# Kernel optimization log

Hardware: AMD Instinct MI355X
Metric: run time of the kernel (lower is better)

Reference implementation:

```python
import jax, jax.numpy as jnp
import numpy as np
from jax import lax


def _pw(x, w, b):
    # pointwise conv1d (kernel_size=1) on [B,C,L]
    return jnp.einsum('oc,bcl->bol', w, x) + b[None, :, None]


def _conv(x, w, b, stride):
    y = lax.conv_general_dilated(x, w, (stride,), 'VALID',
                                 dimension_numbers=('NCH', 'OIH', 'NCH'))
    return y + b[None, :, None]


def setup_inputs() -> dict:
    key = jax.random.key(0)
    ks = jax.random.split(key, 40)
    B, L = 512, 300
    d = {}
    d['x'] = jax.random.randint(ks[0], (B, L), 0, 23)
    def w(k, shape, s=0.1):
        return jax.random.normal(k, shape, dtype=jnp.float32) * s
    d['emb'] = w(ks[1], (23, 128), 1.0)
    d['dr_w'] = w(ks[2], (64, 128)); d['dr_b'] = w(ks[3], (64,), 0.01)
    d['c1_w'] = w(ks[4], (64, 64)); d['c1_b'] = w(ks[5], (64,), 0.01)
    d['c11_w'] = w(ks[6], (64, 64)); d['c11_b'] = w(ks[7], (64,), 0.01)
    d['c12_w'] = w(ks[8], (64, 64)); d['c12_b'] = w(ks[9], (64,), 0.01)
    d['c21_w'] = w(ks[10], (64, 64)); d['c21_b'] = w(ks[11], (64,), 0.01)
    d['c22_w'] = w(ks[12], (64, 64)); d['c22_b'] = w(ks[13], (64,), 0.01)
    d['c31_w'] = w(ks[14], (64, 64)); d['c31_b'] = w(ks[15], (64,), 0.01)
    d['c32_w'] = w(ks[16], (64, 64)); d['c32_b'] = w(ks[17], (64,), 0.01)
    d['c41_w'] = w(ks[18], (64, 64)); d['c41_b'] = w(ks[19], (64,), 0.01)
    d['fc_w'] = w(ks[20], (64, 320)); d['fc_b'] = w(ks[21], (64,), 0.01)
    d['cp1_w'] = w(ks[22], (64, 64, 4)); d['cp1_b'] = w(ks[23], (64,), 0.01)
    d['cp2_w'] = w(ks[24], (64, 64, 5)); d['cp2_b'] = w(ks[25], (64,), 0.01)
    d['wt'] = w(ks[26], (64, 64)); d['wx'] = w(ks[27], (64, 64))
    d['bh'] = w(ks[28], (64,), 0.01)
    d['wa'] = w(ks[29], (64,)); d['ba'] = w(ks[30], (1,), 0.01)
    d['m1_w'] = w(ks[31], (100, 960)); d['m1_b'] = w(ks[32], (100,), 0.01)
    d['m2_w'] = w(ks[33], (1, 100)); d['m2_b'] = w(ks[34], (1,), 0.01)
    return d


def reference(x, emb, dr_w, dr_b, c1_w, c1_b, c11_w, c11_b, c12_w, c12_b,
              c21_w, c21_b, c22_w, c22_b, c31_w, c31_b, c32_w, c32_b,
              c41_w, c41_b, fc_w, fc_b, cp1_w, cp1_b, cp2_w, cp2_b,
              wt, wx, bh, wa, ba, m1_w, m1_b, m2_w, m2_b):
    h = emb[x]                                  # [B,L,128]
    h = jnp.transpose(h, (0, 2, 1))             # [B,128,L]
    r = _pw(h, dr_w, dr_b)                      # [B,64,L]
    r = _pw(r, c1_w, c1_b)
    x2 = _pw(_pw(r, c11_w, c11_b), c12_w, c12_b)
    x3 = _pw(_pw(r, c21_w, c21_b), c22_w, c22_b)
    x4 = _pw(_pw(r, c31_w, c31_b), c32_w, c32_b)
    # MaxPool1d(k=3, s=1, p=1)
    xp = jnp.pad(r, ((0, 0), (0, 0), (1, 1)), constant_values=-jnp.inf)
    p = jnp.maximum(jnp.maximum(xp[:, :, :-2], xp[:, :, 1:-1]), xp[:, :, 2:])
    x5 = _pw(p, c41_w, c41_b)
    h = jnp.concatenate([r, x2, x3, x4, x5], axis=1)   # [B,320,L]
    h = _pw(h, fc_w, fc_b)                             # [B,64,L]
    h = _conv(h, cp1_w, cp1_b, 4)                      # [B,64,75]
    a_in = jnp.transpose(h, (0, 2, 1))                 # [B,75,64]
    # additive attention emission
    qt = a_in @ wt.T                                   # Wt(inputs)
    kx = a_in @ wx.T                                   # Wx(inputs)
    hsc = jnp.tanh(qt[:, :, None, :] + kx[:, None, :, :] + bh)  # [B,75,75,64]
    e = jnp.einsum('bijd,d->bij', hsc, wa) + ba[0]     # [B,75,75]
    a = jax.nn.softmax(e, axis=-1)
    v = jnp.einsum('bij,bjd->bid', a, a_in)            # [B,75,64]
    h = jnp.transpose(v, (0, 2, 1))                    # [B,64,75]
    h = jax.nn.relu(h)
    h = _conv(h, cp2_w, cp2_b, 5)                      # [B,64,15]
    h = h.reshape(h.shape[0], -1)                      # [B,960]
    h = jax.nn.relu(h @ m1_w.T + m1_b)
    return h @ m2_w.T + m2_b                           # [B,1]
```

## Files before the change

### kernel.cpp

```cpp
#include <hip/hip_runtime.h>
#include <hip/hip_bf16.h>

#define DEV __device__ __forceinline__

DEV float fexp2(float x) {
#if __has_builtin(__builtin_amdgcn_exp2f)
  return __builtin_amdgcn_exp2f(x);
#else
  return exp2f(x);
#endif
}
DEV float frcp(float x) {
#if __has_builtin(__builtin_amdgcn_rcpf)
  return __builtin_amdgcn_rcpf(x);
#else
  return 1.0f / x;
#endif
}
DEV float rdlanef(float v, int l) {
#if __has_builtin(__builtin_amdgcn_readlane)
  return __uint_as_float(__builtin_amdgcn_readlane(__float_as_uint(v), l));
#else
  return __shfl(v, l);
#endif
}

#define K_C2LOG2E 2.8853900817779268f

__global__ void __launch_bounds__(256)
prep1(const float* __restrict__ emb,
      const float* __restrict__ dr_w, const float* __restrict__ dr_b,
      const float* __restrict__ c1_w, const float* __restrict__ c1_b,
      const float* __restrict__ w11, const float* __restrict__ b11,
      const float* __restrict__ w12, const float* __restrict__ b12,
      const float* __restrict__ w21, const float* __restrict__ b21,
      const float* __restrict__ w22, const float* __restrict__ b22,
      const float* __restrict__ w31, const float* __restrict__ b31,
      const float* __restrict__ w32, const float* __restrict__ b32,
      const float* __restrict__ fc_w, const float* __restrict__ fc_b,
      const float* __restrict__ c41_w, const float* __restrict__ c41_b,
      float* __restrict__ rt_ext, float* __restrict__ T4,
      float* __restrict__ W5, float* __restrict__ bias_fc)
{
  const int v = blockIdx.x, tid = threadIdx.x;
  if (v < 23) {
    __shared__ float A[64], Rt[64], X2[3][64];
    const int c = tid & 63;
    if (tid < 64) {
      float acc = dr_b[c];
      #pragma unroll 8
      for (int e = 0; e < 32; ++e) {
        const float4 wv = *(const float4*)&dr_w[c * 128 + 4 * e];
        const float4 ev = *(const float4*)&emb[v * 128 + 4 * e];
        acc = fmaf(wv.x, ev.x, acc); acc = fmaf(wv.y, ev.y, acc);
        acc = fmaf(wv.z, ev.z, acc); acc = fmaf(wv.w, ev.w, acc);
      }
      A[c] = acc;
    }
    __syncthreads();
    if (tid < 64) {
      float acc = c1_b[c];
      for (int m = 0; m < 64; ++m) acc = fmaf(c1_w[c * 64 + m], A[m], acc);
      Rt[c] = acc;
      rt_ext[v * 64 + c] = acc;
    }
    for (int br = 0; br < 3; ++br) {
      const float* w1 = (br == 0) ? w11 : (br == 1) ? w21 : w31;
      const float* b1 = (br == 0) ? b11 : (br == 1) ? b21 : b31;
      const float* w2 = (br == 0) ? w12 : (br == 1) ? w22 : w32;
      const float* b2 = (br == 0) ? b12 : (br == 1) ? b22 : b32;
      __syncthreads();
      if (tid < 64) {
        float acc = b1[c];
        for (int m = 0; m < 64; ++m) acc = fmaf(w1[c * 64 + m], Rt[m], acc);
        A[c] = acc;
      }
      __syncthreads();
      if (tid < 64) {
        float acc = b2[c];
        for (int m = 0; m < 64; ++m) acc = fmaf(w2[c * 64 + m], A[m], acc);
        X2[br][c] = acc;
      }
    }
    __syncthreads();
    if (tid < 64) {
      float acc = 0.f;
      for (int m = 0; m < 64; ++m) acc = fmaf(fc_w[c * 320 + m],       Rt[m],    acc);
      for (int m = 0; m < 64; ++m) acc = fmaf(fc_w[c * 320 + 64 + m],  X2[0][m], acc);
      for (int m = 0; m < 64; ++m) acc = fmaf(fc_w[c * 320 + 128 + m], X2[1][m], acc);
      for (int m = 0; m < 64; ++m) acc = fmaf(fc_w[c * 320 + 192 + m], X2[2][m], acc);
      T4[v * 64 + c] = acc;
    }
  } else {
    if (tid < 64) rt_ext[23 * 64 + tid] = -1e30f;
    const int m = tid & 63, c0 = (tid >> 6) * 16;
    float acc[16];
    #pragma unroll
    for (int r = 0; r < 16; ++r) acc[r] = 0.f;
    for (int q = 0; q < 64; ++q) {
      const float w = c41_w[q * 64 + m];
      #pragma unroll
      for (int r = 0; r < 16; ++r)
        acc[r] = fmaf(fc_w[(c0 + r) * 320 + 256 + q], w, acc[r]);
    }
    #pragma unroll
    for (int r = 0; r < 16; ++r) W5[(c0 + r) * 64 + m] = acc[r];
    if (tid < 64) {
      float a2 = fc_b[tid];
      for (int q = 0; q < 64; ++q) a2 = fmaf(fc_w[tid * 320 + 256 + q], c41_b[q], a2);
      bias_fc[tid] = a2;
    }
  }
}

__global__ void __launch_bounds__(256)
tab_T5G(const float* __restrict__ cp1_w, const float* __restrict__ cp1_b,
        const float* __restrict__ T4, const float* __restrict__ W5,
        const float* __restrict__ bias_fc,
        float* __restrict__ T5, float* __restrict__ G, float* __restrict__ bb)
{
  const int k = blockIdx.x, tid = threadIdx.x;
  if (k < 4) {
    __shared__ float slice[64 * 65];
    __shared__ float W5l[64 * 64];
    __shared__ float T4l[23 * 64];
    for (int i = tid; i < 4096; i += 256) {
      const int o = i >> 6, c = i & 63;
      slice[c * 65 + o] = cp1_w[o * 256 + c * 4 + k];
    }
    for (int i = tid; i < 4096; i += 256) W5l[i] = W5[i];
    for (int i = tid; i < 1472; i += 256) T4l[i] = T4[i];
    __syncthreads();
    for (int i = tid; i < 1472; i += 256) {
      const int v = i >> 6, o = i & 63;
      float acc = 0.f;
      for (int c = 0; c < 64; ++c)
        acc = fmaf(slice[c * 65 + o], T4l[v * 64 + c], acc);
      T5[v * 256 + k * 64 + o] = acc;
    }
    for (int i = tid; i < 4096; i += 256) {
      const int m = i >> 6, o = i & 63;
      float acc = 0.f;
      for (int c = 0; c < 64; ++c)
        acc = fmaf(slice[c * 65 + o], W5l[c * 64 + m], acc);
      G[k * 4096 + m * 64 + o] = acc;
    }
  } else {
    if (tid < 64) {
      float acc = cp1_b[tid];
      for (int c = 0; c < 64; ++c) {
        const float* p = &cp1_w[tid * 256 + c * 4];
        acc = fmaf(p[0] + p[1] + p[2] + p[3], bias_fc[c], acc);
      }
      bb[tid] = acc;
    }
  }
}

__global__ void __launch_bounds__(256)
tab_FP5(const float* __restrict__ G, const float* __restrict__ rt_ext,
        float* __restrict__ FP5)
{
  __shared__ float Gl[2][64][64];
  __shared__ float rtl[24 * 64];
  const int tid = threadIdx.x, lane = tid & 63, wave = tid >> 6;
  const int h = blockIdx.x & 1;
  const int vbase = (blockIdx.x >> 1) * 32;
  for (int i = tid; i < 1536; i += 256) rtl[i] = rt_ext[i];
  for (int i = tid; i < 8192; i += 256) ((float*)Gl)[i] = G[h * 8192 + i];
  __syncthreads();
  for (int g = 0; g < 2; ++g) {
    const int j0 = vbase + wave * 8 + g * 4;
    float p[4];
    #pragma unroll
    for (int r = 0; r < 4; ++r) {
      const int v = j0 + r;
      const int a = v / 576, rem = v - a * 576, c = rem / 24, dd = rem - c * 24;
      p[r] = fmaxf(fmaxf(rtl[a * 64 + lane], rtl[c * 64 + lane]), rtl[dd * 64 + lane]);
    }
    float acc[4][2];
    #pragma unroll
    for (int r = 0; r < 4; ++r) { acc[r][0] = 0.f; acc[r][1] = 0.f; }
    #pragma unroll
    for (int m = 0; m < 64; ++m) {
      const float g0 = Gl[0][m][lane], g1 = Gl[1][m][lane];
      #pragma unroll
      for (int r = 0; r < 4; ++r) {
        const float pv = __shfl(p[r], m);
        acc[r][0] = fmaf(g0, pv, acc[r][0]);
        acc[r][1] = fmaf(g1, pv, acc[r][1]);
      }
    }
    #pragma unroll
    for (int r = 0; r < 4; ++r) {
      const int v = j0 + r;
      FP5[v * 256 + (2 * h + 0) * 64 + lane] = acc[r][0];
      FP5[v * 256 + (2 * h + 1) * 64 + lane] = acc[r][1];
    }
  }
}

__global__ void __launch_bounds__(512)
k_main(const int* __restrict__ x,
       const float* __restrict__ wt, const float* __restrict__ wx,
       const float* __restrict__ bh, const float* __restrict__ wa,
       const float* __restrict__ T5, const float* __restrict__ FP5,
       const float* __restrict__ bb, float* __restrict__ vv)
{
  __shared__ int x_lds[304];
  __shared__ __align__(16) float a_in_lds[75 * 64];
  __shared__ __align__(16) float qt_lds[75 * 68];
  __shared__ __align__(16) float kx_lds[75 * 65];
  __shared__ __align__(16) float tail_lds[75 * 12];
  __shared__ float wa_lds[64];

  const int tid = threadIdx.x, lane = tid & 63, wave = tid >> 6;
  const int b = blockIdx.x;

  for (int i = tid; i < 300; i += 512) x_lds[i] = x[b * 300 + i];
  if (tid < 64) wa_lds[tid] = wa[tid];
  __syncthreads();

  {
    const float bbv = bb[lane];
    for (int t = wave; t < 75; t += 8) {
      float acc = bbv;
      #pragma unroll
      for (int k = 0; k < 4; ++k) {
        const int l = 4 * t + k;
        const int xa = (l == 0) ? 23 : x_lds[l - 1];
        const int xd = (l == 299) ? 23 : x_lds[l + 1];
        const int trip = (xa * 576 + x_lds[l] * 24 + xd) * 256;
        acc += T5[x_lds[l] * 256 + k * 64 + lane];
        acc += FP5[trip + k * 64 + lane];
      }
      a_in_lds[t * 64 + lane] = acc;
    }
  }
  __syncthreads();

  {
    float qacc[10], kacc[10];
    #pragma unroll
    for (int r = 0; r < 10; ++r) { qacc[r] = 0.f; kacc[r] = 0.f; }
    for (int c = 0; c < 4; ++c) {
      const float4 t0 = *(const float4*)&wt[lane * 64 + 16 * c];
      const float4 t1 = *(const float4*)&wt[lane * 64 + 16 * c + 4];
      const float4 t2 = *(const float4*)&wt[lane * 64 + 16 * c + 8];
      const float4 t3 = *(const float4*)&wt[lane * 64 + 16 * c + 12];
      const float4 x0 = *(const float4*)&wx[lane * 64 + 16 * c];
      const float4 x1 = *(const float4*)&wx[lane * 64 + 16 * c + 4];
      const float4 x2 = *(const float4*)&wx[lane * 64 + 16 * c + 8];
      const float4 x3 = *(const float4*)&wx[lane * 64 + 16 * c + 12];
      #pragma unroll
      for (int r = 0; r < 10; ++r) {
        const int i = wave + 8 * r;
        if (i < 75) {
          const float* arow = &a_in_lds[i * 64 + 16 * c];
          const float4 a0 = *(const float4*)&arow[0];
          const float4 a1 = *(const float4*)&arow[4];
          const float4 a2 = *(const float4*)&arow[8];
          const float4 a3 = *(const float4*)&arow[12];
          float q = qacc[r], kk = kacc[r];
          q = fmaf(t0.x, a0.x, q); q = fmaf(t0.y, a0.y, q);
          q = fmaf(t0.z, a0.z, q); q = fmaf(t0.w, a0.w, q);
          q = fmaf(t1.x, a1.x, q); q = fmaf(t1.y, a1.y, q);
          q = fmaf(t1.z, a1.z, q); q = fmaf(t1.w, a1.w, q);
          q = fmaf(t2.x, a2.x, q); q = fmaf(t2.y, a2.y, q);
          q = fmaf(t2.z, a2.z, q); q = fmaf(t2.w, a2.w, q);
          q = fmaf(t3.x, a3.x, q); q = fmaf(t3.y, a3.y, q);
          q = fmaf(t3.z, a3.z, q); q = fmaf(t3.w, a3.w, q);
          kk = fmaf(x0.x, a0.x, kk); kk = fmaf(x0.y, a0.y, kk);
          kk = fmaf(x0.z, a0.z, kk); kk = fmaf(x0.w, a0.w, kk);
          kk = fmaf(x1.x, a1.x, kk); kk = fmaf(x1.y, a1.y, kk);
          kk = fmaf(x1.z, a1.z, kk); kk = fmaf(x1.w, a1.w, kk);
          kk = fmaf(x2.x, a2.x, kk); kk = fmaf(x2.y, a2.y, kk);
          kk = fmaf(x2.z, a2.z, kk); kk = fmaf(x2.w, a2.w, kk);
          kk = fmaf(x3.x, a3.x, kk); kk = fmaf(x3.y, a3.y, kk);
          kk = fmaf(x3.z, a3.z, kk); kk = fmaf(x3.w, a3.w, kk);
          qacc[r] = q; kacc[r] = kk;
        }
      }
    }
    const float bhv = bh[lane];
    #pragma unroll
    for (int r = 0; r < 10; ++r) {
      const int i = wave + 8 * r;
      if (i < 75) {
        qt_lds[i * 68 + lane] = (qacc[r] + bhv) * K_C2LOG2E;
        kx_lds[i * 65 + lane] = kacc[r] * K_C2LOG2E;
      }
    }
  }
  __syncthreads();

  for (int idx = tid; idx < 825; idx += 512) {
    const int i = idx / 11, jt = idx - i * 11;
    const float* qrow = &qt_lds[i * 68];
    const float* krow = &kx_lds[(64 + jt) * 65];
    float S = 0.f;
    #pragma unroll 8
    for (int dd = 0; dd < 64; ++dd) {
      const int d = (dd + lane) & 63;
      const float r = frcp(1.f + fexp2(qrow[d] + krow[d]));
      S = fmaf(wa_lds[d], r, S);
    }
    tail_lds[i * 12 + jt] = S;
  }
  __syncthreads();

  float a1r[10], a2r[10];
  #pragma unroll
  for (int r = 0; r < 10; ++r) { a1r[r] = 0.f; a2r[r] = 0.f; }
  {
    const float* krow = &kx_lds[lane * 65];
    #pragma unroll
    for (int r = 0; r < 10; ++r) {
      const int i = wave + 8 * r;
      if (i < 75) {
        float S1 = 0.f;
        #pragma unroll
        for (int q = 0; q < 16; ++q) {
          const float4 q4 = *(const float4*)&qt_lds[i * 68 + 4 * q];
          const float4 w4 = *(const float4*)&wa_lds[4 * q];
          float rr;
          rr = frcp(1.f + fexp2(q4.x + krow[4 * q + 0])); S1 = fmaf(w4.x, rr, S1);
          rr = frcp(1.f + fexp2(q4.y + krow[4 * q + 1])); S1 = fmaf(w4.y, rr, S1);
          rr = frcp(1.f + fexp2(q4.z + krow[4 * q + 2])); S1 = fmaf(w4.z, rr, S1);
          rr = frcp(1.f + fexp2(q4.w + krow[4 * q + 3])); S1 = fmaf(w4.w, rr, S1);
        }
        const float z1 = S1 * (-K_C2LOG2E);
        const float zt = (lane < 11) ? tail_lds[i * 12 + lane] * (-K_C2LOG2E) : -1e30f;
        float m = fmaxf(z1, zt);
        #pragma unroll
        for (int off = 32; off; off >>= 1) m = fmaxf(m, __shfl_xor(m, off));
        const float p1 = fexp2(z1 - m);
        const float p2 = (lane < 11) ? fexp2(zt - m) : 0.f;
        float s = p1 + p2;
        #pragma unroll
        for (int off = 32; off; off >>= 1) s += __shfl_xor(s, off);
        const float inv = frcp(s);
        a1r[r] = p1 * inv;
        a2r[r] = p2 * inv;
      }
    }
  }

  {
    float acc[10];
    #pragma unroll
    for (int r = 0; r < 10; ++r) acc[r] = 0.f;
    for (int j = 0; j < 64; ++j) {
      const float ajo = a_in_lds[j * 64 + lane];
      #pragma unroll
      for (int r = 0; r < 10; ++r)
        acc[r] = fmaf(rdlanef(a1r[r], j), ajo, acc[r]);
    }
    for (int j = 0; j < 11; ++j) {
      const float ajo = a_in_lds[(64 + j) * 64 + lane];
      #pragma unroll
      for (int r = 0; r < 10; ++r)
        acc[r] = fmaf(rdlanef(a2r[r], j), ajo, acc[r]);
    }
    #pragma unroll
    for (int r = 0; r < 10; ++r) {
      const int i = wave + 8 * r;
      if (i < 75) vv[b * 4800 + i * 64 + lane] = fmaxf(acc[r], 0.f);
    }
  }
}

__global__ void __launch_bounds__(256)
k_tail(const float* __restrict__ vv,
       const float* __restrict__ cp2_w, const float* __restrict__ cp2_b,
       const float* __restrict__ m1_w, const float* __restrict__ m1_b,
       const float* __restrict__ m2_w, const float* __restrict__ m2_b,
       float* __restrict__ out)
{
  __shared__ __align__(16) float vv_lds[75 * 65];
  __shared__ float g_lds[960];
  __shared__ float y_lds[100];
  const int tid = threadIdx.x, lane = tid & 63, wave = tid >> 6;
  const int b = blockIdx.x;

  for (int idx = tid; idx < 4800; idx += 256) {
    const int i = idx >> 6, d = idx & 63;
    vv_lds[i * 65 + d] = vv[b * 4800 + idx];
  }
  __syncthreads();
  for (int idx = tid; idx < 960; idx += 256) {
    const int s = idx >> 6, o = idx & 63;
    float acc = cp2_b[o];
    for (int c = 0; c < 64; ++c) {
      const float* wrow = &cp2_w[(o * 64 + c) * 5];
      const float* vrow = &vv_lds[5 * s * 65 + c];
      #pragma unroll
      for (int k = 0; k < 5; ++k)
        acc = fmaf(wrow[k], vrow[k * 65], acc);
    }
    g_lds[o * 15 + s] = acc;
  }
  __syncthreads();

  for (int u = wave; u < 100; u += 4) {
    float acc0 = 0.f;
    #pragma unroll
    for (int it = 0; it < 15; ++it) {
      const int n = it * 64 + lane;
      acc0 = fmaf(m1_w[u * 960 + n], g_lds[n], acc0);
    }
    #pragma unroll
    for (int off = 32; off; off >>= 1) acc0 += __shfl_xor(acc0, off);
    if (lane == 0) y_lds[u] = fmaxf(acc0 + m1_b[u], 0.f);
  }
  __syncthreads();
  if (wave == 0) {
    float s = y_lds[lane] * m2_w[lane];
    if (lane < 36) s = fmaf(y_lds[lane + 64], m2_w[lane + 64], s);
    #pragma unroll
    for (int off = 32; off; off >>= 1) s += __shfl_xor(s, off);
    if (lane == 0) out[b] = s + m2_b[0];
  }
}

extern "C" void kernel_launch(void* const* d_in, const int* in_sizes, int n_in,
                              void* d_out, int out_size, void* d_ws, size_t ws_size,
                              hipStream_t stream) {
  (void)in_sizes; (void)n_in; (void)out_size; (void)ws_size;
  const int*   x     = (const int*)  d_in[0];
  const float* emb   = (const float*)d_in[1];
  const float* dr_w  = (const float*)d_in[2];
  const float* dr_b  = (const float*)d_in[3];
  const float* c1_w  = (const float*)d_in[4];
  const float* c1_b  = (const float*)d_in[5];
  const float* c11_w = (const float*)d_in[6];
  const float* c11_b = (const float*)d_in[7];
  const float* c12_w = (const float*)d_in[8];
  const float* c12_b = (const float*)d_in[9];
  const float* c21_w = (const float*)d_in[10];
  const float* c21_b = (const float*)d_in[11];
  const float* c22_w = (const float*)d_in[12];
  const float* c22_b = (const float*)d_in[13];
  const float* c31_w = (const float*)d_in[14];
  const float* c31_b = (const float*)d_in[15];
  const float* c32_w = (const float*)d_in[16];
  const float* c32_b = (const float*)d_in[17];
  const float* c41_w = (const float*)d_in[18];
  const float* c41_b = (const float*)d_in[19];
  const float* fc_w  = (const float*)d_in[20];
  const float* fc_b  = (const float*)d_in[21];
  const float* cp1_w = (const float*)d_in[22];
  const float* cp1_b = (const float*)d_in[23];
  const float* cp2_w = (const float*)d_in[24];
  const float* cp2_b = (const float*)d_in[25];
  const float* wt    = (const float*)d_in[26];
  const float* wx    = (const float*)d_in[27];
  const float* bh    = (const float*)d_in[28];
  const float* wa    = (const float*)d_in[29];
  const float* m1_w  = (const float*)d_in[31];
  const float* m1_b  = (const float*)d_in[32];
  const float* m2_w  = (const float*)d_in[33];
  const float* m2_b  = (const float*)d_in[34];
  float* out = (float*)d_out;

  float* ws      = (float*)d_ws;
  float* rt_ext  = ws;
  float* T5      = ws + 1536;
  float* bb      = ws + 7424;
  float* G       = ws + 7488;
  float* bias_fc = ws + 23872;
  float* T4      = ws + 28352;
  float* W5      = ws + 29824;
  float* FP5     = ws + 33920;
  float* vv      = ws + 3572864;

  prep1  <<<24, 256, 0, stream>>>(emb, dr_w, dr_b, c1_w, c1_b,
                                  c11_w, c11_b, c12_w, c12_b,
                                  c21_w, c21_b, c22_w, c22_b,
                                  c31_w, c31_b, c32_w, c32_b,
                                  fc_w, fc_b, c41_w, c41_b,
                                  rt_ext, T4, W5, bias_fc);
  tab_T5G<<<5, 256, 0, stream>>>(cp1_w, cp1_b, T4, W5, bias_fc, T5, G, bb);
  tab_FP5<<<864, 256, 0, stream>>>(G, rt_ext, FP5);
  k_main <<<512, 512, 0, stream>>>(x, wt, wx, bh, wa, T5, FP5, bb, vv);
  k_tail <<<512, 256, 0, stream>>>(vv, cp2_w, cp2_b, m1_w, m1_b, m2_w, m2_b, out);
}
```

Baseline: 385.6 us.

## Interchange attention score loops for kx reuse and batch two samples per tail block

In k_main, the main attention score loop is interchanged so each lane loads its kx row as float4 once per 16-wide chunk and reuses it across all 10 query rows. The kx row stride is padded from 65 to 68 so those float4 loads are aligned. k_tail now handles two batch elements per block, so each m1_w load is shared by two dot products and the grid is halved. Costs are higher register pressure from 10 live accumulators in k_main, and serialized conv work per tail block.

After: 327.6 us. 1.18x faster.

```diff
diff --git a/kernel.cpp b/kernel.cpp
--- a/kernel.cpp
+++ b/kernel.cpp
@@ -210,7 +210,7 @@
   __shared__ int x_lds[304];
   __shared__ __align__(16) float a_in_lds[75 * 64];
   __shared__ __align__(16) float qt_lds[75 * 68];
-  __shared__ __align__(16) float kx_lds[75 * 65];
+  __shared__ __align__(16) float kx_lds[75 * 68];
   __shared__ __align__(16) float tail_lds[75 * 12];
   __shared__ float wa_lds[64];
 
@@ -288,7 +288,7 @@
       const int i = wave + 8 * r;
       if (i < 75) {
         qt_lds[i * 68 + lane] = (qacc[r] + bhv) * K_C2LOG2E;
-        kx_lds[i * 65 + lane] = kacc[r] * K_C2LOG2E;
+        kx_lds[i * 68 + lane] = kacc[r] * K_C2LOG2E;
       }
     }
   }
@@ -297,7 +297,7 @@
   for (int idx = tid; idx < 825; idx += 512) {
     const int i = idx / 11, jt = idx - i * 11;
     const float* qrow = &qt_lds[i * 68];
-    const float* krow = &kx_lds[(64 + jt) * 65];
+    const float* krow = &kx_lds[(64 + jt) * 68];
     float S = 0.f;
     #pragma unroll 8
     for (int dd = 0; dd < 64; ++dd) {
@@ -309,40 +309,47 @@
   }
   __syncthreads();
 
+  float S1[10];
+  #pragma unroll
+  for (int r = 0; r < 10; ++r) S1[r] = 0.f;
+  #pragma unroll
+  for (int q = 0; q < 16; ++q) {
+    const float4 k4 = *(const float4*)&kx_lds[lane * 68 + 4 * q];
+    const float4 w4 = *(const float4*)&wa_lds[4 * q];
+    #pragma unroll
+    for (int r = 0; r < 10; ++r) {
+      const int i = wave + 8 * r;
+      if (i < 75) {
+        const float4 q4 = *(const float4*)&qt_lds[i * 68 + 4 * q];
+        float rr;
+        rr = frcp(1.f + fexp2(q4.x + k4.x)); S1[r] = fmaf(w4.x, rr, S1[r]);
+        rr = frcp(1.f + fexp2(q4.y + k4.y)); S1[r] = fmaf(w4.y, rr, S1[r]);
+        rr = frcp(1.f + fexp2(q4.z + k4.z)); S1[r] = fmaf(w4.z, rr, S1[r]);
+        rr = frcp(1.f + fexp2(q4.w + k4.w)); S1[r] = fmaf(w4.w, rr, S1[r]);
+      }
+    }
+  }
+
   float a1r[10], a2r[10];
   #pragma unroll
   for (int r = 0; r < 10; ++r) { a1r[r] = 0.f; a2r[r] = 0.f; }
-  {
-    const float* krow = &kx_lds[lane * 65];
-    #pragma unroll
-    for (int r = 0; r < 10; ++r) {
-      const int i = wave + 8 * r;
-      if (i < 75) {
-        float S1 = 0.f;
-        #pragma unroll
-        for (int q = 0; q < 16; ++q) {
-          const float4 q4 = *(const float4*)&qt_lds[i * 68 + 4 * q];
-          const float4 w4 = *(const float4*)&wa_lds[4 * q];
-          float rr;
-          rr = frcp(1.f + fexp2(q4.x + krow[4 * q + 0])); S1 = fmaf(w4.x, rr, S1);
-          rr = frcp(1.f + fexp2(q4.y + krow[4 * q + 1])); S1 = fmaf(w4.y, rr, S1);
-          rr = frcp(1.f + fexp2(q4.z + krow[4 * q + 2])); S1 = fmaf(w4.z, rr, S1);
-          rr = frcp(1.f + fexp2(q4.w + krow[4 * q + 3])); S1 = fmaf(w4.w, rr, S1);
-        }
-        const float z1 = S1 * (-K_C2LOG2E);
-        const float zt = (lane < 11) ? tail_lds[i * 12 + lane] * (-K_C2LOG2E) : -1e30f;
-        float m = fmaxf(z1, zt);
-        #pragma unroll
-        for (int off = 32; off; off >>= 1) m = fmaxf(m, __shfl_xor(m, off));
-        const float p1 = fexp2(z1 - m);
-        const float p2 = (lane < 11) ? fexp2(zt - m) : 0.f;
-        float s = p1 + p2;
-        #pragma unroll
-        for (int off = 32; off; off >>= 1) s += __shfl_xor(s, off);
-        const float inv = frcp(s);
-        a1r[r] = p1 * inv;
-        a2r[r] = p2 * inv;
-      }
+  #pragma unroll
+  for (int r = 0; r < 10; ++r) {
+    const int i = wave + 8 * r;
+    if (i < 75) {
+      const float z1 = S1[r] * (-K_C2LOG2E);
+      const float zt = (lane < 11) ? tail_lds[i * 12 + lane] * (-K_C2LOG2E) : -1e30f;
+      float m = fmaxf(z1, zt);
+      #pragma unroll
+      for (int off = 32; off; off >>= 1) m = fmaxf(m, __shfl_xor(m, off));
+      const float p1 = fexp2(z1 - m);
+      const float p2 = (lane < 11) ? fexp2(zt - m) : 0.f;
+      float s = p1 + p2;
+      #pragma unroll
+      for (int off = 32; off; off >>= 1) s += __shfl_xor(s, off);
+      const float inv = frcp(s);
+      a1r[r] = p1 * inv;
+      a2r[r] = p2 * inv;
     }
   }
 
@@ -378,48 +385,62 @@
        float* __restrict__ out)
 {
   __shared__ __align__(16) float vv_lds[75 * 65];
-  __shared__ float g_lds[960];
-  __shared__ float y_lds[100];
+  __shared__ float g_lds[2][960];
+  __shared__ float y_lds[2][100];
   const int tid = threadIdx.x, lane = tid & 63, wave = tid >> 6;
-  const int b = blockIdx.x;
-
-  for (int idx = tid; idx < 4800; idx += 256) {
-    const int i = idx >> 6, d = idx & 63;
-    vv_lds[i * 65 + d] = vv[b * 4800 + idx];
-  }
-  __syncthreads();
-  for (int idx = tid; idx < 960; idx += 256) {
-    const int s = idx >> 6, o = idx & 63;
-    float acc = cp2_b[o];
-    for (int c = 0; c < 64; ++c) {
-      const float* wrow = &cp2_w[(o * 64 + c) * 5];
-      const float* vrow = &vv_lds[5 * s * 65 + c];
-      #pragma unroll
-      for (int k = 0; k < 5; ++k)
-        acc = fmaf(wrow[k], vrow[k * 65], acc);
-    }
-    g_lds[o * 15 + s] = acc;
+  const int b0 = blockIdx.x * 2;
+
+  for (int q = 0; q < 2; ++q) {
+    const int b = b0 + q;
+    __syncthreads();
+    for (int idx = tid; idx < 4800; idx += 256) {
+      const int i = idx >> 6, d = idx & 63;
+      vv_lds[i * 65 + d] = vv[b * 4800 + idx];
+    }
+    __syncthreads();
+    for (int idx = tid; idx < 960; idx += 256) {
+      const int o = idx / 15, s = idx % 15;
+      float acc = cp2_b[o];
+      for (int c = 0; c < 64; ++c) {
+        const float* wrow = &cp2_w[(o * 64 + c) * 5];
+        const float* vrow = &vv_lds[5 * s * 65 + c];
+        #pragma unroll
+        for (int k = 0; k < 5; ++k)
+          acc = fmaf(wrow[k], vrow[k * 65], acc);
+      }
+      g_lds[q][idx] = acc;
+    }
   }
   __syncthreads();
 
   for (int u = wave; u < 100; u += 4) {
-    float acc0 = 0.f;
+    float acc0 = 0.f, acc1 = 0.f;
     #pragma unroll
     for (int it = 0; it < 15; ++it) {
       const int n = it * 64 + lane;
-      acc0 = fmaf(m1_w[u * 960 + n], g_lds[n], acc0);
-    }
-    #pragma unroll
-    for (int off = 32; off; off >>= 1) acc0 += __shfl_xor(acc0, off);
-    if (lane == 0) y_lds[u] = fmaxf(acc0 + m1_b[u], 0.f);
-  }
-  __syncthreads();
-  if (wave == 0) {
-    float s = y_lds[lane] * m2_w[lane];
-    if (lane < 36) s = fmaf(y_lds[lane + 64], m2_w[lane + 64], s);
+      const float w = m1_w[u * 960 + n];
+      acc0 = fmaf(w, g_lds[0][n], acc0);
+      acc1 = fmaf(w, g_lds[1][n], acc1);
+    }
+    #pragma unroll
+    for (int off = 32; off; off >>= 1) {
+      acc0 += __shfl_xor(acc0, off);
+      acc1 += __shfl_xor(acc1, off);
+    }
+    if (lane == 0) {
+      const float mb = m1_b[u];
+      y_lds[0][u] = fmaxf(acc0 + mb, 0.f);
+      y_lds[1][u] = fmaxf(acc1 + mb, 0.f);
+    }
+  }
+  __syncthreads();
+  if (wave < 2) {
+    const int q = wave;
+    float s = y_lds[q][lane] * m2_w[lane];
+    if (lane < 36) s = fmaf(y_lds[q][lane + 64], m2_w[lane + 64], s);
     #pragma unroll
     for (int off = 32; off; off >>= 1) s += __shfl_xor(s, off);
-    if (lane == 0) out[b] = s + m2_b[0];
+    if (lane == 0) out[b0 + q] = s + m2_b[0];
   }
 }
 
@@ -483,5 +504,5 @@
   tab_T5G<<<5, 256, 0, stream>>>(cp1_w, cp1_b, T4, W5, bias_fc, T5, G, bb);
   tab_FP5<<<864, 256, 0, stream>>>(G, rt_ext, FP5);
   k_main <<<512, 512, 0, stream>>>(x, wt, wx, bh, wa, T5, FP5, bb, vv);
-  k_tail <<<512, 256, 0, stream>>>(vv, cp2_w, cp2_b, m1_w, m1_b, m2_w, m2_b, out);
-}
+  k_tail <<<256, 256, 0, stream>>>(vv, cp2_w, cp2_b, m1_w, m1_b, m2_w, m2_b, out);
+}
```
